# Optimization experiments

Measured on AMD Instinct MI355X. Metric: run time of the kernel, lower is better.

The kernel has to match this reference:

```python
import jax, jax.numpy as jnp
import numpy as np

N_NODES = 100000
N_EDGES = 1000000
N_FEAT = 136
HIDDEN = 64
N_CLASSES = 2
NUM_GRAPHS = 512


def setup_inputs() -> dict:
    key = jax.random.key(0)
    ks = jax.random.split(key, 8)
    x = jax.random.normal(ks[0], (N_NODES, N_FEAT), dtype=jnp.float32)
    edge_index = jax.random.randint(ks[1], (2, N_EDGES), 0, N_NODES, dtype=jnp.int64)
    batch = jnp.sort(jax.random.randint(ks[2], (N_NODES,), 0, NUM_GRAPHS, dtype=jnp.int64))
    W1 = jax.random.normal(ks[3], (N_FEAT, HIDDEN), dtype=jnp.float32) * (1.0 / np.sqrt(N_FEAT))
    b1 = jnp.zeros((HIDDEN,), dtype=jnp.float32)
    W2 = jax.random.normal(ks[4], (HIDDEN, HIDDEN), dtype=jnp.float32) * (1.0 / np.sqrt(HIDDEN))
    b2 = jnp.zeros((HIDDEN,), dtype=jnp.float32)
    Wout = jax.random.normal(ks[5], (HIDDEN, N_CLASSES), dtype=jnp.float32) * (1.0 / np.sqrt(HIDDEN))
    bout = jnp.zeros((N_CLASSES,), dtype=jnp.float32)
    return {"x": x, "edge_index": edge_index, "batch": batch,
            "W1": W1, "b1": b1, "W2": W2, "b2": b2, "Wout": Wout, "bout": bout}


def _gcn_conv(x, src, dst, W, b, n_nodes):
    # GCNConv: D^{-1/2} (A+I) D^{-1/2} X W + b (self-loops already appended in src/dst)
    h = x @ W                                           # [N, out]
    ones = jnp.ones(src.shape, dtype=h.dtype)
    deg = jax.ops.segment_sum(ones, dst, num_segments=n_nodes)  # in-degree incl. self-loop
    dinv = jnp.where(deg > 0, jax.lax.rsqrt(deg), 0.0)
    norm = dinv[src] * dinv[dst]                        # [E]
    msg = h[src] * norm[:, None]                        # gather + normalize
    out = jax.ops.segment_sum(msg, dst, num_segments=n_nodes)   # scatter-add
    return out + b


def reference(x, edge_index, batch, W1, b1, W2, b2, Wout, bout):
    n = x.shape[0]
    loops = jnp.arange(n, dtype=edge_index.dtype)
    src = jnp.concatenate([edge_index[0], loops])
    dst = jnp.concatenate([edge_index[1], loops])

    h = jax.nn.relu(_gcn_conv(x, src, dst, W1, b1, n))
    # dropout p=0.5 is identity in eval mode
    h = jax.nn.relu(_gcn_conv(h, src, dst, W2, b2, n))

    # global_mean_pool over batch segments
    sums = jax.ops.segment_sum(h, batch, num_segments=NUM_GRAPHS)       # [G, H]
    counts = jax.ops.segment_sum(jnp.ones((n,), h.dtype), batch, num_segments=NUM_GRAPHS)
    pooled = sums / jnp.maximum(counts, 1.0)[:, None]

    return pooled @ Wout + bout                                         # [G, C]
```

## Files before the change

### kernel.cpp

```cpp
#include <hip/hip_runtime.h>
#include <hip/hip_bf16.h>

#define N_NODES   100000
#define N_EDGES   1000000
#define N_FEAT    136
#define HIDDEN    64
#define N_CLASSES 2
#define NUM_GRAPHS 512

#define NP_PAD    100352
#define SCAN_BLKS 98

#define EPW       128
#define NWAVE     7813
#define E_PAD     (NWAVE * EPW)
#define SEG_BLOCKS ((NWAVE + 3) / 4)

#define K1_4 (N_FEAT / 4)
#define K2_4 (HIDDEN / 4)

#define K1PAD 160
#define K2PAD 72

#define NB_E  ((N_EDGES + 255) / 256)
#define NB_SC ((N_EDGES / 4 + 255) / 256)

typedef unsigned short ushort_t;
typedef __attribute__((ext_vector_type(8))) short bf16x8;
typedef __attribute__((ext_vector_type(4))) float f32x4;
typedef __attribute__((ext_vector_type(4))) int i32x4;
typedef __attribute__((ext_vector_type(4))) unsigned short u16x4;

__device__ __forceinline__ ushort_t f2b(float v) {
    unsigned b = __float_as_uint(v);
    return (ushort_t)((b + 0x7FFF + ((b >> 16) & 1)) >> 16);
}
__device__ __forceinline__ float b2f(ushort_t u) {
    return __uint_as_float(((unsigned)u) << 16);
}
__device__ __forceinline__ unsigned pack2(float a, float b) {
    return (unsigned)f2b(a) | ((unsigned)f2b(b) << 16);
}

__global__ __launch_bounds__(256) void hist_kernel(const int* __restrict__ dst,
                                                   int* __restrict__ cnt,
                                                   ushort_t* __restrict__ rank,
                                                   const int* __restrict__ batch,
                                                   int* __restrict__ gstart) {
    if (blockIdx.x >= NB_E) {
        int g = (blockIdx.x - NB_E) * 256 + threadIdx.x;
        if (g <= NUM_GRAPHS) {
            int lo = 0, hi = N_NODES;
            while (lo < hi) {
                int mid = (lo + hi) >> 1;
                if (batch[mid] < g) lo = mid + 1; else hi = mid;
            }
            gstart[g] = lo;
        }
        return;
    }
    int e = blockIdx.x * 256 + threadIdx.x;
    if (e < N_EDGES) {
        int d = __builtin_nontemporal_load(&dst[e]);
        int r = atomicAdd(&cnt[d], 1);
        rank[e] = (ushort_t)r;
    }
}

__global__ __launch_bounds__(256) void scan1_kernel(const int* __restrict__ cnt,
                                                    int* __restrict__ row_ptr,
                                                    int* __restrict__ partials) {
    __shared__ int sd[256];
    int b = blockIdx.x, t = threadIdx.x;
    int i0 = b * 1024 + t * 4;
    int c0 = (i0 + 0 < N_NODES) ? cnt[i0 + 0] : 0;
    int c1 = (i0 + 1 < N_NODES) ? cnt[i0 + 1] : 0;
    int c2 = (i0 + 2 < N_NODES) ? cnt[i0 + 2] : 0;
    int c3 = (i0 + 3 < N_NODES) ? cnt[i0 + 3] : 0;
    int tsum = c0 + c1 + c2 + c3;
    sd[t] = tsum;
    __syncthreads();
    for (int off = 1; off < 256; off <<= 1) {
        int v = (t >= off) ? sd[t - off] : 0;
        __syncthreads();
        sd[t] += v;
        __syncthreads();
    }
    int excl = sd[t] - tsum;
    row_ptr[i0 + 0] = excl;
    row_ptr[i0 + 1] = excl + c0;
    row_ptr[i0 + 2] = excl + c0 + c1;
    row_ptr[i0 + 3] = excl + c0 + c1 + c2;
    if (t == 255) partials[b] = sd[255];
}

__global__ __launch_bounds__(128) void scan2_kernel(int* __restrict__ partials) {
    __shared__ int sd[128];
    int t = threadIdx.x;
    int v = (t < SCAN_BLKS) ? partials[t] : 0;
    sd[t] = v;
    __syncthreads();
    for (int off = 1; off < 128; off <<= 1) {
        int u = (t >= off) ? sd[t - off] : 0;
        __syncthreads();
        sd[t] += u;
        __syncthreads();
    }
    partials[t] = sd[t] - v;
}

__global__ __launch_bounds__(256) void scan3_kernel(int* __restrict__ row_ptr,
                                                    const int* __restrict__ cnt,
                                                    const int* __restrict__ partials,
                                                    int* __restrict__ dst_sorted,
                                                    int* __restrict__ csr_src,
                                                    float* __restrict__ dinv) {
    int i = blockIdx.x * 256 + threadIdx.x;
    if (i < N_NODES) {
        int v = row_ptr[i] + partials[i >> 10];
        int deg = cnt[i];
        row_ptr[i] = v;
        dinv[i] = rsqrtf((float)(deg + 1));
        for (int j = v; j < v + deg; ++j) dst_sorted[j] = i;
    }
    if (i == N_NODES) {
        row_ptr[N_NODES] = N_EDGES;
        for (int j = N_EDGES; j < E_PAD; ++j) {
            dst_sorted[j] = N_NODES;
            csr_src[j] = 0;
        }
    }
}

__global__ __launch_bounds__(256) void scatter_kernel(const int* __restrict__ src,
                                                      const int* __restrict__ dst,
                                                      const ushort_t* __restrict__ rank,
                                                      const int* __restrict__ row_ptr,
                                                      int* __restrict__ csr_src) {
    int e0 = (blockIdx.x * 256 + threadIdx.x) * 4;
    if (e0 >= N_EDGES) return;
    i32x4 s4 = __builtin_nontemporal_load((const i32x4*)&src[e0]);
    i32x4 d4 = __builtin_nontemporal_load((const i32x4*)&dst[e0]);
    u16x4 r4 = *(const u16x4*)&rank[e0];
    int p0 = row_ptr[d4.x] + (int)r4.x;
    int p1 = row_ptr[d4.y] + (int)r4.y;
    int p2 = row_ptr[d4.z] + (int)r4.z;
    int p3 = row_ptr[d4.w] + (int)r4.w;
    csr_src[p0] = s4.x;
    csr_src[p1] = s4.y;
    csr_src[p2] = s4.z;
    csr_src[p3] = s4.w;
}

__global__ __launch_bounds__(256) void mm1_kernel(const float* __restrict__ x,
                                                  const float* __restrict__ W1,
                                                  const float* __restrict__ dinv,
                                                  ushort_t* __restrict__ tpb,
                                                  float* __restrict__ agg) {
    __shared__ ushort_t xsb[64 * K1PAD];
    __shared__ ushort_t wtb[64 * K1PAD];
    __shared__ float    dsv[64];
    int t = threadIdx.x;
    int n0 = blockIdx.x * 64;
    {
        for (int i = t; i < 64 * 16; i += 256) {
            int r = i >> 4, c = i & 15;
            int n = n0 + r;
            if (n < N_NODES)
                ((float4*)agg)[n * 16 + c] = make_float4(0.f, 0.f, 0.f, 0.f);
        }
        const float4* x4 = (const float4*)x;
        for (int i = t; i < 64 * K1_4; i += 256) {
            int r = i / K1_4, c = i % K1_4;
            int n = n0 + r; if (n >= N_NODES) n = N_NODES - 1;
            float4 v = x4[(long long)n * K1_4 + c];
            *(uint2*)&xsb[r * K1PAD + 4 * c] =
                make_uint2(pack2(v.x, v.y), pack2(v.z, v.w));
        }
        for (int i = t; i < 64 * 12; i += 256) {
            int r = i / 12, c = i % 12;
            *(unsigned*)&xsb[r * K1PAD + N_FEAT + 2 * c] = 0;
        }
        for (int i = t; i < N_FEAT * HIDDEN; i += 256) {
            int n = i & 63, k = i >> 6;
            wtb[n * K1PAD + k] = f2b(W1[i]);
        }
        for (int i = t; i < 64 * 12; i += 256) {
            int n = i / 12, c = i % 12;
            *(unsigned*)&wtb[n * K1PAD + N_FEAT + 2 * c] = 0;
        }
        if (t < 64) {
            int n = n0 + t; if (n >= N_NODES) n = N_NODES - 1;
            dsv[t] = dinv[n];
        }
    }
    __syncthreads();
    int w = t >> 6, lane = t & 63;
    int quad = lane >> 4, l16 = lane & 15;
    f32x4 acc[4] = {{0,0,0,0},{0,0,0,0},{0,0,0,0},{0,0,0,0}};
#pragma unroll
    for (int kc = 0; kc < K1PAD / 32; ++kc) {
        bf16x8 a = *(const bf16x8*)&xsb[(w * 16 + l16) * K1PAD + kc * 32 + quad * 8];
#pragma unroll
        for (int nt = 0; nt < 4; ++nt) {
            bf16x8 b = *(const bf16x8*)&wtb[(nt * 16 + l16) * K1PAD + kc * 32 + quad * 8];
            acc[nt] = __builtin_amdgcn_mfma_f32_16x16x32_bf16(a, b, acc[nt], 0, 0, 0);
        }
    }
#pragma unroll
    for (int r = 0; r < 4; ++r) {
        int nl = w * 16 + quad * 4 + r;
        int node = n0 + nl;
        if (node < N_NODES) {
            float di = dsv[nl];
#pragma unroll
            for (int nt = 0; nt < 4; ++nt)
                tpb[node * 64 + nt * 16 + l16] = f2b(acc[nt][r] * di);
        }
    }
}

__global__ __launch_bounds__(256) void mm2_kernel(float* __restrict__ agg,
                                                  ushort_t* __restrict__ tpb,
                                                  const float* __restrict__ W2,
                                                  const float* __restrict__ dinv,
                                                  const float* __restrict__ bias) {
    __shared__ ushort_t hsb[64 * K2PAD];
    __shared__ ushort_t wtb[64 * K2PAD];
    __shared__ float    dsv[64];
    __shared__ float    bsv[64];
    int t = threadIdx.x;
    int n0 = blockIdx.x * 64;
    if (t < 64) {
        int n = n0 + t; if (n >= N_NODES) n = N_NODES - 1;
        dsv[t] = dinv[n];
        bsv[t] = bias[t];
    }
    __syncthreads();
    {
        for (int i = t; i < HIDDEN * HIDDEN; i += 256) {
            int n = i & 63, k = i >> 6;
            wtb[n * K2PAD + k] = f2b(W2[i]);
        }
        for (int i = t; i < 64 * 4; i += 256) {
            int n = i / 4, c = i % 4;
            *(unsigned*)&wtb[n * K2PAD + HIDDEN + 2 * c] = 0;
        }
        for (int i = t; i < 64 * 16; i += 256) {
            int r = i >> 4, c = i & 15;
            int n_raw = n0 + r;
            int n = (n_raw < N_NODES) ? n_raw : N_NODES - 1;
            float4 va = ((const float4*)agg)[n * 16 + c];
            uint2 ut = *(const uint2*)&tpb[n * 64 + c * 4];
            float di = dsv[r];
            float s0 = b2f((ushort_t)(ut.x & 0xffff));
            float s1 = b2f((ushort_t)(ut.x >> 16));
            float s2 = b2f((ushort_t)(ut.y & 0xffff));
            float s3 = b2f((ushort_t)(ut.y >> 16));
            float h0 = fmaxf(fmaf(va.x + s0, di, bsv[c * 4 + 0]), 0.f);
            float h1 = fmaxf(fmaf(va.y + s1, di, bsv[c * 4 + 1]), 0.f);
            float h2 = fmaxf(fmaf(va.z + s2, di, bsv[c * 4 + 2]), 0.f);
            float h3 = fmaxf(fmaf(va.w + s3, di, bsv[c * 4 + 3]), 0.f);
            *(uint2*)&hsb[r * K2PAD + 4 * c] = make_uint2(pack2(h0, h1), pack2(h2, h3));
            if (n_raw < N_NODES)
                ((float4*)agg)[n * 16 + c] = make_float4(0.f, 0.f, 0.f, 0.f);
        }
        for (int i = t; i < 64 * 4; i += 256) {
            int r = i / 4, c = i % 4;
            *(unsigned*)&hsb[r * K2PAD + HIDDEN + 2 * c] = 0;
        }
    }
    __syncthreads();
    int w = t >> 6, lane = t & 63;
    int quad = lane >> 4, l16 = lane & 15;
    f32x4 acc[4] = {{0,0,0,0},{0,0,0,0},{0,0,0,0},{0,0,0,0}};
#pragma unroll
    for (int kc = 0; kc < 2; ++kc) {
        bf16x8 a = *(const bf16x8*)&hsb[(w * 16 + l16) * K2PAD + kc * 32 + quad * 8];
#pragma unroll
        for (int nt = 0; nt < 4; ++nt) {
            bf16x8 b = *(const bf16x8*)&wtb[(nt * 16 + l16) * K2PAD + kc * 32 + quad * 8];
            acc[nt] = __builtin_amdgcn_mfma_f32_16x16x32_bf16(a, b, acc[nt], 0, 0, 0);
        }
    }
#pragma unroll
    for (int r = 0; r < 4; ++r) {
        int nl = w * 16 + quad * 4 + r;
        int node = n0 + nl;
        if (node < N_NODES) {
            float di = dsv[nl];
#pragma unroll
            for (int nt = 0; nt < 4; ++nt)
                tpb[node * 64 + nt * 16 + l16] = f2b(acc[nt][r] * di);
        }
    }
}

__global__ __launch_bounds__(256, 4) void edge_seg_kernel(const int* __restrict__ csr_src,
                                                          const int* __restrict__ dst_sorted,
                                                          const ushort_t* __restrict__ tpb,
                                                          float* __restrict__ agg) {
    int lane = threadIdx.x & 63;
    int wid  = (blockIdx.x * 256 + threadIdx.x) >> 6;
    if (wid >= NWAVE) return;
    int e0 = wid * EPW;

    int sv0 = csr_src[e0 + lane],      sv1 = csr_src[e0 + 64 + lane];
    int dv0 = dst_sorted[e0 + lane],   dv1 = dst_sorted[e0 + 64 + lane];

    float acc = 0.0f;
    int dprev = __builtin_amdgcn_readlane(dv0, 0);
    int nflush = 0;
#pragma unroll
    for (int j = 0; j < 8; ++j) {
        int svj = (j < 4) ? sv0 : sv1;
        int dvj = (j < 4) ? dv0 : dv1;
        int base = (j * 16) & 63;
        int ss[16], dd[16];
#pragma unroll
        for (int k = 0; k < 16; ++k) {
            ss[k] = __builtin_amdgcn_readlane(svj, base + k);
            dd[k] = __builtin_amdgcn_readlane(dvj, base + k);
        }
        float vv[16];
#pragma unroll
        for (int k = 0; k < 16; ++k) vv[k] = b2f(tpb[ss[k] * 64 + lane]);
#pragma unroll
        for (int k = 0; k < 16; ++k) {
            if (dd[k] != dprev) {
                if (nflush == 0) atomicAdd(&agg[dprev * 64 + lane], acc);
                else             agg[dprev * 64 + lane] = acc;
                ++nflush;
                acc = 0.0f;
                dprev = dd[k];
            }
            acc += vv[k];
        }
    }
    atomicAdd(&agg[dprev * 64 + lane], acc);
}

__global__ __launch_bounds__(256) void gpool_kernel(const float* __restrict__ agg,
                                                    const ushort_t* __restrict__ tpb,
                                                    const float* __restrict__ dinv,
                                                    const float* __restrict__ bias,
                                                    const int* __restrict__ gstart,
                                                    const float* __restrict__ Wout,
                                                    const float* __restrict__ bout,
                                                    float* __restrict__ out) {
    __shared__ float red[4][64];
    int lane = threadIdx.x & 63;
    int w = threadIdx.x >> 6;
    int g = blockIdx.x;
    int s = gstart[g], e = gstart[g + 1];
    float b = bias[lane];
    float acc = 0.0f;
    for (int n = s + w; n < e; n += 4) {
        int idx = n * 64 + lane;
        acc += fmaxf(fmaf(agg[idx] + b2f(tpb[idx]), dinv[n], b), 0.0f);
    }
    red[w][lane] = acc;
    __syncthreads();
    if (threadIdx.x < 64) {
        float tot = red[0][lane] + red[1][lane] + red[2][lane] + red[3][lane];
        float p = tot / fmaxf((float)(e - s), 1.0f);
        float c0 = p * Wout[lane * N_CLASSES + 0];
        float c1 = p * Wout[lane * N_CLASSES + 1];
#pragma unroll
        for (int off = 32; off > 0; off >>= 1) {
            c0 += __shfl_down(c0, off);
            c1 += __shfl_down(c1, off);
        }
        if (lane == 0) {
            out[g * N_CLASSES + 0] = c0 + bout[0];
            out[g * N_CLASSES + 1] = c1 + bout[1];
        }
    }
}

extern "C" void kernel_launch(void* const* d_in, const int* in_sizes, int n_in,
                              void* d_out, int out_size, void* d_ws, size_t ws_size,
                              hipStream_t stream) {
    const float* x     = (const float*)d_in[0];
    const int*   ei    = (const int*)d_in[1];
    const int*   batch = (const int*)d_in[2];
    const float* W1    = (const float*)d_in[3];
    const float* b1    = (const float*)d_in[4];
    const float* W2    = (const float*)d_in[5];
    const float* b2    = (const float*)d_in[6];
    const float* Wout  = (const float*)d_in[7];
    const float* bout  = (const float*)d_in[8];
    float* out = (float*)d_out;

    const int* src = ei;
    const int* dst = ei + N_EDGES;

    char* p = (char*)d_ws;
    int*      row_ptr   = (int*)p;      p += (NP_PAD + 256) * sizeof(int);
    int*      cnt       = (int*)p;      p += NP_PAD * sizeof(int);
    int*      partials  = (int*)p;      p += 256 * sizeof(int);
    int*      gstart    = (int*)p;      p += (NUM_GRAPHS + 64) * sizeof(int);
    int*      csr_src   = (int*)p;      p += (size_t)E_PAD * sizeof(int);
    int*      dst_sorted= (int*)p;      p += (size_t)E_PAD * sizeof(int);
    float*    dinv      = (float*)p;    p += NP_PAD * sizeof(float);
    ushort_t* tpb       = (ushort_t*)p; p += (size_t)N_NODES * HIDDEN * sizeof(ushort_t);
    float*    agg       = (float*)p;    p += (size_t)(N_NODES + 1) * HIDDEN * sizeof(float);
    ushort_t* rank16    = (ushort_t*)agg;

    const int NB_MM = (N_NODES + 63) / 64;

    hipMemsetAsync(cnt, 0, NP_PAD * sizeof(int), stream);
    hist_kernel<<<NB_E + 3, 256, 0, stream>>>(dst, cnt, rank16, batch, gstart);
    scan1_kernel<<<SCAN_BLKS, 256, 0, stream>>>(cnt, row_ptr, partials);
    scan2_kernel<<<1, 128, 0, stream>>>(partials);
    scan3_kernel<<<NP_PAD / 256 + 1, 256, 0, stream>>>(row_ptr, cnt, partials,
                                                       dst_sorted, csr_src, dinv);
    scatter_kernel<<<NB_SC, 256, 0, stream>>>(src, dst, rank16, row_ptr, csr_src);

    mm1_kernel<<<NB_MM, 256, 0, stream>>>(x, W1, dinv, tpb, agg);
    edge_seg_kernel<<<SEG_BLOCKS, 256, 0, stream>>>(csr_src, dst_sorted, tpb, agg);

    mm2_kernel<<<NB_MM, 256, 0, stream>>>(agg, tpb, W2, dinv, b1);
    edge_seg_kernel<<<SEG_BLOCKS, 256, 0, stream>>>(csr_src, dst_sorted, tpb, agg);

    gpool_kernel<<<NUM_GRAPHS, 256, 0, stream>>>(agg, tpb, dinv, b2, gstart,
                                                 Wout, bout, out);
}
```

Before: 283.4 us.

## Fuse histogram with first matmul and move source degree scaling into edge gather

```diff
diff --git a/kernel.cpp b/kernel.cpp
--- a/kernel.cpp
+++ b/kernel.cpp
@@ -22,8 +22,11 @@
 #define K1PAD 160
 #define K2PAD 72
 
-#define NB_E  ((N_EDGES + 255) / 256)
-#define NB_SC ((N_EDGES / 4 + 255) / 256)
+#define NB_E    ((N_EDGES + 255) / 256)
+#define NB_SC   ((N_EDGES / 4 + 255) / 256)
+#define NB_HIST (NB_E + 3)
+#define NB_MM   ((N_NODES + 63) / 64)
+#define FUSED_GRID 5474
 
 typedef unsigned short ushort_t;
 typedef __attribute__((ext_vector_type(8))) short bf16x8;
@@ -42,28 +45,88 @@
     return (unsigned)f2b(a) | ((unsigned)f2b(b) << 16);
 }
 
-__global__ __launch_bounds__(256) void hist_kernel(const int* __restrict__ dst,
-                                                   int* __restrict__ cnt,
-                                                   ushort_t* __restrict__ rank,
-                                                   const int* __restrict__ batch,
-                                                   int* __restrict__ gstart) {
-    if (blockIdx.x >= NB_E) {
-        int g = (blockIdx.x - NB_E) * 256 + threadIdx.x;
-        if (g <= NUM_GRAPHS) {
-            int lo = 0, hi = N_NODES;
-            while (lo < hi) {
-                int mid = (lo + hi) >> 1;
-                if (batch[mid] < g) lo = mid + 1; else hi = mid;
+__global__ __launch_bounds__(256) void fused_hist_mm1_kernel(
+        const int* __restrict__ dst, int* __restrict__ cnt,
+        ushort_t* __restrict__ rank,
+        const int* __restrict__ batch, int* __restrict__ gstart,
+        const float* __restrict__ x, const float* __restrict__ W1,
+        ushort_t* __restrict__ tpb) {
+    __shared__ ushort_t xsb[64 * K1PAD];
+    __shared__ ushort_t wtb[64 * K1PAD];
+    int t = threadIdx.x;
+    int gq = blockIdx.x / 7, gr = blockIdx.x % 7;
+
+    if (gr >= 2) {
+        int hb = gq * 5 + (gr - 2);
+        if (hb >= NB_HIST) return;
+        if (hb >= NB_E) {
+            int g = (hb - NB_E) * 256 + t;
+            if (g <= NUM_GRAPHS) {
+                int lo = 0, hi = N_NODES;
+                while (lo < hi) {
+                    int mid = (lo + hi) >> 1;
+                    if (batch[mid] < g) lo = mid + 1; else hi = mid;
+                }
+                gstart[g] = lo;
             }
-            gstart[g] = lo;
+            return;
+        }
+        int e = hb * 256 + t;
+        if (e < N_EDGES) {
+            int d = __builtin_nontemporal_load(&dst[e]);
+            int r = atomicAdd(&cnt[d], 1);
+            __builtin_nontemporal_store((ushort_t)r, &rank[e]);
         }
         return;
     }
-    int e = blockIdx.x * 256 + threadIdx.x;
-    if (e < N_EDGES) {
-        int d = __builtin_nontemporal_load(&dst[e]);
-        int r = atomicAdd(&cnt[d], 1);
-        rank[e] = (ushort_t)r;
+
+    int mb = gq * 2 + gr;
+    if (mb >= NB_MM) return;
+    int n0 = mb * 64;
+    {
+        const float4* x4 = (const float4*)x;
+        for (int i = t; i < 64 * K1_4; i += 256) {
+            int r = i / K1_4, c = i % K1_4;
+            int n = n0 + r; if (n >= N_NODES) n = N_NODES - 1;
+            float4 v = x4[(long long)n * K1_4 + c];
+            *(uint2*)&xsb[r * K1PAD + 4 * c] =
+                make_uint2(pack2(v.x, v.y), pack2(v.z, v.w));
+        }
+        for (int i = t; i < 64 * 12; i += 256) {
+            int r = i / 12, c = i % 12;
+            *(unsigned*)&xsb[r * K1PAD + N_FEAT + 2 * c] = 0;
+        }
+        for (int i = t; i < N_FEAT * HIDDEN; i += 256) {
+            int n = i & 63, k = i >> 6;
+            wtb[n * K1PAD + k] = f2b(W1[i]);
+        }
+        for (int i = t; i < 64 * 12; i += 256) {
+            int n = i / 12, c = i % 12;
+            *(unsigned*)&wtb[n * K1PAD + N_FEAT + 2 * c] = 0;
+        }
+    }
+    __syncthreads();
+    int w = t >> 6, lane = t & 63;
+    int quad = lane >> 4, l16 = lane & 15;
+    f32x4 acc[4] = {{0,0,0,0},{0,0,0,0},{0,0,0,0},{0,0,0,0}};
+#pragma unroll
+    for (int kc = 0; kc < K1PAD / 32; ++kc) {
+        bf16x8 a = *(const bf16x8*)&xsb[(w * 16 + l16) * K1PAD + kc * 32 + quad * 8];
+#pragma unroll
+        for (int nt = 0; nt < 4; ++nt) {
+            bf16x8 b = *(const bf16x8*)&wtb[(nt * 16 + l16) * K1PAD + kc * 32 + quad * 8];
+            acc[nt] = __builtin_amdgcn_mfma_f32_16x16x32_bf16(a, b, acc[nt], 0, 0, 0);
+        }
+    }
+#pragma unroll
+    for (int r = 0; r < 4; ++r) {
+        int nl = w * 16 + quad * 4 + r;
+        int node = n0 + nl;
+        if (node < N_NODES) {
+#pragma unroll
+            for (int nt = 0; nt < 4; ++nt)
+                tpb[node * 64 + nt * 16 + l16] = f2b(acc[nt][r]);
+        }
     }
 }
 
@@ -152,74 +215,6 @@
     csr_src[p3] = s4.w;
 }
 
-__global__ __launch_bounds__(256) void mm1_kernel(const float* __restrict__ x,
-                                                  const float* __restrict__ W1,
-                                                  const float* __restrict__ dinv,
-                                                  ushort_t* __restrict__ tpb,
-                                                  float* __restrict__ agg) {
-    __shared__ ushort_t xsb[64 * K1PAD];
-    __shared__ ushort_t wtb[64 * K1PAD];
-    __shared__ float    dsv[64];
-    int t = threadIdx.x;
-    int n0 = blockIdx.x * 64;
-    {
-        for (int i = t; i < 64 * 16; i += 256) {
-            int r = i >> 4, c = i & 15;
-            int n = n0 + r;
-            if (n < N_NODES)
-                ((float4*)agg)[n * 16 + c] = make_float4(0.f, 0.f, 0.f, 0.f);
-        }
-        const float4* x4 = (const float4*)x;
-        for (int i = t; i < 64 * K1_4; i += 256) {
-            int r = i / K1_4, c = i % K1_4;
-            int n = n0 + r; if (n >= N_NODES) n = N_NODES - 1;
-            float4 v = x4[(long long)n * K1_4 + c];
-            *(uint2*)&xsb[r * K1PAD + 4 * c] =
-                make_uint2(pack2(v.x, v.y), pack2(v.z, v.w));
-        }
-        for (int i = t; i < 64 * 12; i += 256) {
-            int r = i / 12, c = i % 12;
-            *(unsigned*)&xsb[r * K1PAD + N_FEAT + 2 * c] = 0;
-        }
-        for (int i = t; i < N_FEAT * HIDDEN; i += 256) {
-            int n = i & 63, k = i >> 6;
-            wtb[n * K1PAD + k] = f2b(W1[i]);
-        }
-        for (int i = t; i < 64 * 12; i += 256) {
-            int n = i / 12, c = i % 12;
-            *(unsigned*)&wtb[n * K1PAD + N_FEAT + 2 * c] = 0;
-        }
-        if (t < 64) {
-            int n = n0 + t; if (n >= N_NODES) n = N_NODES - 1;
-            dsv[t] = dinv[n];
-        }
-    }
-    __syncthreads();
-    int w = t >> 6, lane = t & 63;
-    int quad = lane >> 4, l16 = lane & 15;
-    f32x4 acc[4] = {{0,0,0,0},{0,0,0,0},{0,0,0,0},{0,0,0,0}};
-#pragma unroll
-    for (int kc = 0; kc < K1PAD / 32; ++kc) {
-        bf16x8 a = *(const bf16x8*)&xsb[(w * 16 + l16) * K1PAD + kc * 32 + quad * 8];
-#pragma unroll
-        for (int nt = 0; nt < 4; ++nt) {
-            bf16x8 b = *(const bf16x8*)&wtb[(nt * 16 + l16) * K1PAD + kc * 32 + quad * 8];
-            acc[nt] = __builtin_amdgcn_mfma_f32_16x16x32_bf16(a, b, acc[nt], 0, 0, 0);
-        }
-    }
-#pragma unroll
-    for (int r = 0; r < 4; ++r) {
-        int nl = w * 16 + quad * 4 + r;
-        int node = n0 + nl;
-        if (node < N_NODES) {
-            float di = dsv[nl];
-#pragma unroll
-            for (int nt = 0; nt < 4; ++nt)
-                tpb[node * 64 + nt * 16 + l16] = f2b(acc[nt][r] * di);
-        }
-    }
-}
-
 __global__ __launch_bounds__(256) void mm2_kernel(float* __restrict__ agg,
                                                   ushort_t* __restrict__ tpb,
                                                   const float* __restrict__ W2,
@@ -253,10 +248,10 @@
             float4 va = ((const float4*)agg)[n * 16 + c];
             uint2 ut = *(const uint2*)&tpb[n * 64 + c * 4];
             float di = dsv[r];
-            float s0 = b2f((ushort_t)(ut.x & 0xffff));
-            float s1 = b2f((ushort_t)(ut.x >> 16));
-            float s2 = b2f((ushort_t)(ut.y & 0xffff));
-            float s3 = b2f((ushort_t)(ut.y >> 16));
+            float s0 = b2f((ushort_t)(ut.x & 0xffff)) * di;
+            float s1 = b2f((ushort_t)(ut.x >> 16)) * di;
+            float s2 = b2f((ushort_t)(ut.y & 0xffff)) * di;
+            float s3 = b2f((ushort_t)(ut.y >> 16)) * di;
             float h0 = fmaxf(fmaf(va.x + s0, di, bsv[c * 4 + 0]), 0.f);
             float h1 = fmaxf(fmaf(va.y + s1, di, bsv[c * 4 + 1]), 0.f);
             float h2 = fmaxf(fmaf(va.z + s2, di, bsv[c * 4 + 2]), 0.f);
@@ -296,9 +291,11 @@
     }
 }
 
+template<bool SCALE_SRC>
 __global__ __launch_bounds__(256, 4) void edge_seg_kernel(const int* __restrict__ csr_src,
                                                           const int* __restrict__ dst_sorted,
                                                           const ushort_t* __restrict__ tpb,
+                                                          const float* __restrict__ dinv,
                                                           float* __restrict__ agg) {
     int lane = threadIdx.x & 63;
     int wid  = (blockIdx.x * 256 + threadIdx.x) >> 6;
@@ -324,7 +321,11 @@
         }
         float vv[16];
 #pragma unroll
-        for (int k = 0; k < 16; ++k) vv[k] = b2f(tpb[ss[k] * 64 + lane]);
+        for (int k = 0; k < 16; ++k) {
+            float v = b2f(tpb[ss[k] * 64 + lane]);
+            if (SCALE_SRC) v *= dinv[ss[k]];
+            vv[k] = v;
+        }
 #pragma unroll
         for (int k = 0; k < 16; ++k) {
             if (dd[k] != dprev) {
@@ -407,21 +408,24 @@
     float*    agg       = (float*)p;    p += (size_t)(N_NODES + 1) * HIDDEN * sizeof(float);
     ushort_t* rank16    = (ushort_t*)agg;
 
-    const int NB_MM = (N_NODES + 63) / 64;
-
     hipMemsetAsync(cnt, 0, NP_PAD * sizeof(int), stream);
-    hist_kernel<<<NB_E + 3, 256, 0, stream>>>(dst, cnt, rank16, batch, gstart);
+    fused_hist_mm1_kernel<<<FUSED_GRID, 256, 0, stream>>>(dst, cnt, rank16,
+                                                          batch, gstart,
+                                                          x, W1, tpb);
     scan1_kernel<<<SCAN_BLKS, 256, 0, stream>>>(cnt, row_ptr, partials);
     scan2_kernel<<<1, 128, 0, stream>>>(partials);
     scan3_kernel<<<NP_PAD / 256 + 1, 256, 0, stream>>>(row_ptr, cnt, partials,
                                                        dst_sorted, csr_src, dinv);
     scatter_kernel<<<NB_SC, 256, 0, stream>>>(src, dst, rank16, row_ptr, csr_src);
 
-    mm1_kernel<<<NB_MM, 256, 0, stream>>>(x, W1, dinv, tpb, agg);
-    edge_seg_kernel<<<SEG_BLOCKS, 256, 0, stream>>>(csr_src, dst_sorted, tpb, agg);
+    hipMemsetAsync(agg, 0, (size_t)(N_NODES + 1) * HIDDEN * sizeof(float), stream);
+
+    edge_seg_kernel<true><<<SEG_BLOCKS, 256, 0, stream>>>(csr_src, dst_sorted,
+                                                          tpb, dinv, agg);
 
     mm2_kernel<<<NB_MM, 256, 0, stream>>>(agg, tpb, W2, dinv, b1);
-    edge_seg_kernel<<<SEG_BLOCKS, 256, 0, stream>>>(csr_src, dst_sorted, tpb, agg);
+    edge_seg_kernel<false><<<SEG_BLOCKS, 256, 0, stream>>>(csr_src, dst_sorted,
+                                                           tpb, dinv, agg);
 
     gpool_kernel<<<NUM_GRAPHS, 256, 0, stream>>>(agg, tpb, dinv, b2, gstart,
                                                  Wout, bout, out);
```

Result: faster. 264.0 us (-6.8%).
